# Performance work log

Hardware: AMD Instinct MI355X
Metric: run time of the kernel (lower is better)

The kernel has to match this reference:

```python
import math
import jax, jax.numpy as jnp
import numpy as np

HEADS = 8


def setup_inputs() -> dict:
    key = jax.random.key(0)
    k1, k2, k3 = jax.random.split(key, 3)
    b, n, a, dim = 1, 256, 256, 512
    init_scale = 0.02
    x = jax.random.normal(k1, (b, n, a, dim), dtype=jnp.float32)
    w_qkv = jax.random.normal(k2, (dim, 3 * dim), dtype=jnp.float32) * init_scale
    b_qkv = jnp.zeros((3 * dim,), dtype=jnp.float32)
    w_proj = jax.random.normal(k3, (dim, dim), dtype=jnp.float32) * init_scale
    b_proj = jnp.zeros((dim,), dtype=jnp.float32)
    return {"x": x, "w_qkv": w_qkv, "b_qkv": b_qkv, "w_proj": w_proj, "b_proj": b_proj}


def reference(x, w_qkv, b_qkv, w_proj, b_proj):
    b, n, a, dim = x.shape
    dh = dim // HEADS
    scale = 1.0 / math.sqrt(math.sqrt(dh))
    qkv = jnp.einsum('bnad,de->bnae', x, w_qkv) + b_qkv  # [b,n,a,3*dim]
    qkv = qkv.reshape(b, n, a, HEADS, 3 * dh)
    q, k, v = jnp.split(qkv, 3, axis=-1)  # each [b,n,a,h,dh]
    # scores over the 'a' axis, independent per (b, n, head)
    sim = jnp.einsum('bnihd,bnjhd->bnhij', q * scale, k * scale)
    attn = jax.nn.softmax(sim, axis=-1)
    out = jnp.einsum('bnhij,bnjhd->bnihd', attn, v).reshape(b, n, a, dim)
    return jnp.einsum('bnad,de->bnae', out, w_proj) + b_proj
```

## Files before the change

### kernel.cpp

```cpp
#include <hip/hip_runtime.h>

typedef unsigned short u16;
typedef unsigned int u32;
typedef __bf16 bf16x8 __attribute__((ext_vector_type(8)));
typedef float f32x4 __attribute__((ext_vector_type(4)));

__device__ __forceinline__ u16 f2b(float f) {
  u32 u = __builtin_bit_cast(u32, f);
  u32 r = (u + 0x7fffu + ((u >> 16) & 1u)) >> 16;
  return (u16)r;
}
__device__ __forceinline__ bf16x8 ld_frag(const u16* p) {
  uint4 v = *(const uint4*)p;
  return __builtin_bit_cast(bf16x8, v);
}
__device__ __forceinline__ void async_lds16(const u16* g, u16* lds) {
  __builtin_amdgcn_global_load_lds(
      (const __attribute__((address_space(1))) void*)g,
      (__attribute__((address_space(3))) void*)lds, 16, 0, 0);
}
__device__ __forceinline__ void wait_lds() { __builtin_amdgcn_s_waitcnt(0xc07f); }

__global__ __launch_bounds__(256) void convert_f32_bf16(const float* __restrict__ in,
                                                        u16* __restrict__ out) {
  long i = ((long)blockIdx.x * 256 + threadIdx.x) * 8;
  float4 a = *(const float4*)(in + i);
  float4 b = *(const float4*)(in + i + 4);
  union { uint4 v; u16 e[8]; } u;
  u.e[0] = f2b(a.x); u.e[1] = f2b(a.y); u.e[2] = f2b(a.z); u.e[3] = f2b(a.w);
  u.e[4] = f2b(b.x); u.e[5] = f2b(b.y); u.e[6] = f2b(b.z); u.e[7] = f2b(b.w);
  *(uint4*)(out + i) = u.v;
}

__global__ __launch_bounds__(256) void transpose_w(const float* __restrict__ W,
                                                   u16* __restrict__ Wt,
                                                   int K, int N) {
  __shared__ alignas(16) u16 T[64][80];
  const int n0 = blockIdx.x * 64, k0 = blockIdx.y * 64;
  const int t = threadIdx.x;
  {
    int kk = t >> 3, c = t & 7;
#pragma unroll
    for (int rr = 0; rr < 2; ++rr) {
      int kr = kk + rr * 32;
      const float* src = W + (long)(k0 + kr) * N + n0 + c * 8;
      float4 a = *(const float4*)src;
      float4 b = *(const float4*)(src + 4);
      u16* dst = &T[kr][c * 8];
      dst[0] = f2b(a.x); dst[1] = f2b(a.y); dst[2] = f2b(a.z); dst[3] = f2b(a.w);
      dst[4] = f2b(b.x); dst[5] = f2b(b.y); dst[6] = f2b(b.z); dst[7] = f2b(b.w);
    }
  }
  __syncthreads();
  {
    int nn = t >> 3, kc = t & 7;
#pragma unroll
    for (int rr = 0; rr < 2; ++rr) {
      int nr = nn + rr * 32;
      union { uint4 v; u16 e[8]; } u;
#pragma unroll
      for (int i = 0; i < 8; ++i) u.e[i] = T[kc * 8 + i][nr];
      *(uint4*)(Wt + (long)(n0 + nr) * K + k0 + kc * 8) = u.v;
    }
  }
}

template <bool OUT_F32>
__global__ __launch_bounds__(256) void gemm_bt(const u16* __restrict__ A,
                                               const u16* __restrict__ Bt,
                                               const float* __restrict__ bias,
                                               void* __restrict__ Cv,
                                               int M, int N, int K) {
  __shared__ alignas(16) u16 As[128 * 32];
  __shared__ alignas(16) u16 Bs[128 * 32];
  const int tid = threadIdx.x;
  const int lane = tid & 63, wave = tid >> 6;
  const int quad = lane >> 4, ln = lane & 15;
  const int wm = wave & 1, wn = wave >> 1;
  const long m0 = (long)blockIdx.y * 128;
  const long n0 = (long)blockIdx.x * 128;

  f32x4 zero = {0.f, 0.f, 0.f, 0.f};
  f32x4 acc[4][4];
#pragma unroll
  for (int i = 0; i < 4; ++i)
#pragma unroll
    for (int j = 0; j < 4; ++j) acc[i][j] = zero;

  const int c1 = tid + 256;
  const int rowA0 = tid >> 2, colA0 = (tid & 3) * 8;
  const int rowA1 = c1 >> 2, colA1 = (c1 & 3) * 8;
  u16* ldsA0 = &As[wave * 512];
  u16* ldsA1 = &As[2048 + wave * 512];
  u16* ldsB0 = &Bs[wave * 512];
  u16* ldsB1 = &Bs[2048 + wave * 512];

  for (int k0 = 0; k0 < K; k0 += 32) {
    async_lds16(A + (m0 + rowA0) * K + k0 + colA0, ldsA0);
    async_lds16(A + (m0 + rowA1) * K + k0 + colA1, ldsA1);
    async_lds16(Bt + (n0 + rowA0) * K + k0 + colA0, ldsB0);
    async_lds16(Bt + (n0 + rowA1) * K + k0 + colA1, ldsB1);
    __builtin_amdgcn_s_waitcnt(0x0f70);
    __syncthreads();
    bf16x8 af[4], bfr[4];
#pragma unroll
    for (int mt = 0; mt < 4; ++mt)
      af[mt] = ld_frag(&As[(wm * 64 + mt * 16 + ln) * 32 + quad * 8]);
#pragma unroll
    for (int nt = 0; nt < 4; ++nt)
      bfr[nt] = ld_frag(&Bs[(wn * 64 + nt * 16 + ln) * 32 + quad * 8]);
#pragma unroll
    for (int mt = 0; mt < 4; ++mt)
#pragma unroll
      for (int nt = 0; nt < 4; ++nt)
        acc[mt][nt] = __builtin_amdgcn_mfma_f32_16x16x32_bf16(af[mt], bfr[nt], acc[mt][nt], 0, 0, 0);
    __syncthreads();
  }

  if (OUT_F32) {
#pragma unroll
    for (int nt = 0; nt < 4; ++nt) {
      long coln = n0 + wn * 64 + nt * 16 + ln;
      float bv = bias[coln];
#pragma unroll
      for (int mt = 0; mt < 4; ++mt) {
        long rowb = m0 + wm * 64 + mt * 16 + quad * 4;
#pragma unroll
        for (int r = 0; r < 4; ++r)
          ((float*)Cv)[(rowb + r) * N + coln] = acc[mt][nt][r] + bv;
      }
    }
  } else {
    u16* buf = (wm == 0) ? As : Bs;
    for (int mt = 0; mt < 4; ++mt) {
      __syncthreads();
#pragma unroll
      for (int nt = 0; nt < 4; ++nt) {
        long coln = n0 + wn * 64 + nt * 16 + ln;
        float bv = bias[coln];
#pragma unroll
        for (int r = 0; r < 4; ++r)
          buf[(quad * 4 + r) * 136 + wn * 64 + nt * 16 + ln] = f2b(acc[mt][nt][r] + bv);
      }
      __syncthreads();
#pragma unroll
      for (int it = 0; it < 2; ++it) {
        int cid = it * 256 + tid;
        int bufi = cid >> 8, row = (cid >> 4) & 15, ch = cid & 15;
        const u16* sb = bufi ? Bs : As;
        uint4 v = *(const uint4*)&sb[row * 136 + ch * 8];
        *(uint4*)&((u16*)Cv)[(m0 + (long)bufi * 64 + mt * 16 + row) * N + n0 + ch * 8] = v;
      }
    }
  }
}

__global__ __launch_bounds__(256, 2) void attn_fused(const u16* __restrict__ qkv,
                                                     u16* __restrict__ out) {
  __shared__ alignas(16) u16 Ks[256 * 64];
  __shared__ alignas(16) u16 Vt[64 * 256];
  const int h = blockIdx.x;
  const long n = blockIdx.y;
  const int tid = threadIdx.x;
  const int lane = tid & 63, wave = tid >> 6;
  const int quad = lane >> 4, ln = lane & 15;
  const u16* base = qkv + (n * 256) * 1536 + h * 192;

  auto stageK = [&]() {
    int c = tid & 7, jb = tid >> 3;
#pragma unroll
    for (int rr = 0; rr < 8; ++rr) {
      int j = jb + rr * 32;
      uint4 v = *(const uint4*)(base + (long)j * 1536 + 64 + c * 8);
      *(uint4*)&Ks[j * 64 + ((c ^ (j & 7)) * 8)] = v;
    }
  };
  stageK();
  {
    int p = tid & 7, jb = tid >> 3;
#pragma unroll
    for (int rr = 0; rr < 8; ++rr) {
      int j = jb + rr * 32;
      union { uint4 v; u16 e[8]; } u;
      u.v = *(const uint4*)(base + (long)j * 1536 + 128 + p * 8);
      int cj = j >> 3, jl = j & 7;
#pragma unroll
      for (int i = 0; i < 8; ++i) {
        int d = p * 8 + i;
        int key = (p ^ i) & 7;
        Vt[d * 256 + ((cj ^ key) * 8) + jl] = u.e[i];
      }
    }
  }
  __syncthreads();

  u16* Pw = &Ks[wave * 2176];
  f32x4 zero = {0.f, 0.f, 0.f, 0.f};

  for (int s = 0; s < 2; ++s) {
    const int row0 = wave * 64 + s * 32;
    bf16x8 qa[2][2];
#pragma unroll
    for (int mt = 0; mt < 2; ++mt)
#pragma unroll
      for (int kc = 0; kc < 2; ++kc)
        qa[mt][kc] = ld_frag(base + (long)(row0 + mt * 16 + ln) * 1536 + kc * 32 + quad * 8);

    f32x4 sacc[2][16];
#pragma unroll
    for (int mt = 0; mt < 2; ++mt)
#pragma unroll
      for (int jt = 0; jt < 16; ++jt) sacc[mt][jt] = zero;

#pragma unroll
    for (int jt = 0; jt < 16; ++jt) {
#pragma unroll
      for (int kc = 0; kc < 2; ++kc) {
        bf16x8 kb = ld_frag(&Ks[(jt * 16 + ln) * 64 + (((kc * 4 + quad) ^ (ln & 7)) * 8)]);
        sacc[0][jt] = __builtin_amdgcn_mfma_f32_16x16x32_bf16(qa[0][kc], kb, sacc[0][jt], 0, 0, 0);
        sacc[1][jt] = __builtin_amdgcn_mfma_f32_16x16x32_bf16(qa[1][kc], kb, sacc[1][jt], 0, 0, 0);
      }
    }
    __syncthreads();

#pragma unroll
    for (int mt = 0; mt < 2; ++mt) {
      float linv[4];
#pragma unroll
      for (int r = 0; r < 4; ++r) {
        float mx = -3.0e38f;
#pragma unroll
        for (int jt = 0; jt < 16; ++jt) mx = fmaxf(mx, sacc[mt][jt][r]);
        mx = fmaxf(mx, __shfl_xor(mx, 1));
        mx = fmaxf(mx, __shfl_xor(mx, 2));
        mx = fmaxf(mx, __shfl_xor(mx, 4));
        mx = fmaxf(mx, __shfl_xor(mx, 8));
        float l = 0.f;
#pragma unroll
        for (int jt = 0; jt < 16; ++jt) {
          float p = __expf((sacc[mt][jt][r] - mx) * 0.125f);
          sacc[mt][jt][r] = p;
          l += p;
        }
        l += __shfl_xor(l, 1);
        l += __shfl_xor(l, 2);
        l += __shfl_xor(l, 4);
        l += __shfl_xor(l, 8);
        linv[r] = 1.0f / l;
      }

      f32x4 oacc[4];
#pragma unroll
      for (int dt = 0; dt < 4; ++dt) oacc[dt] = zero;
#pragma unroll
      for (int jh = 0; jh < 2; ++jh) {
#pragma unroll
        for (int jl = 0; jl < 8; ++jl) {
          int jt = jh * 8 + jl;
#pragma unroll
          for (int r = 0; r < 4; ++r)
            Pw[(quad * 4 + r) * 136 + jl * 16 + ln] = f2b(sacc[mt][jt][r]);
        }
        wait_lds();
#pragma unroll
        for (int jcl = 0; jcl < 4; ++jcl) {
          bf16x8 pa = ld_frag(&Pw[ln * 136 + jcl * 32 + quad * 8]);
          int cjb = (jh * 4 + jcl) * 4 + quad;
#pragma unroll
          for (int dt = 0; dt < 4; ++dt) {
            int d = dt * 16 + ln;
            int key = ((d >> 3) ^ d) & 7;
            bf16x8 vb = ld_frag(&Vt[d * 256 + ((cjb ^ key) * 8)]);
            oacc[dt] = __builtin_amdgcn_mfma_f32_16x16x32_bf16(pa, vb, oacc[dt], 0, 0, 0);
          }
        }
      }
#pragma unroll
      for (int dt = 0; dt < 4; ++dt)
#pragma unroll
        for (int r = 0; r < 4; ++r)
          Pw[(quad * 4 + r) * 136 + dt * 16 + ln] = f2b(oacc[dt][r] * linv[r]);
      wait_lds();
#pragma unroll
      for (int it = 0; it < 2; ++it) {
        int cid = it * 64 + lane;
        int row = cid >> 3, ch = cid & 7;
        uint4 v = *(const uint4*)&Pw[row * 136 + ch * 8];
        *(uint4*)&out[(n * 256 + row0 + mt * 16 + row) * 512 + h * 64 + ch * 8] = v;
      }
    }
    __syncthreads();
    if (s == 0) {
      stageK();
      __syncthreads();
    }
  }
}

extern "C" void kernel_launch(void* const* d_in, const int* in_sizes, int n_in,
                              void* d_out, int out_size, void* d_ws, size_t ws_size,
                              hipStream_t stream) {
  const float* x      = (const float*)d_in[0];
  const float* w_qkv  = (const float*)d_in[1];
  const float* b_qkv  = (const float*)d_in[2];
  const float* w_proj = (const float*)d_in[3];
  const float* b_proj = (const float*)d_in[4];
  float* out = (float*)d_out;

  char* ws = (char*)d_ws;
  u16* xb   = (u16*)ws;
  u16* qkv  = (u16*)(ws + 67108864L);
  u16* attn = (u16*)(ws + 67108864L + 201326592L);
  u16* Wt1  = (u16*)(ws + 67108864L + 201326592L + 67108864L);
  u16* Wt2  = Wt1 + 1536 * 512;

  convert_f32_bf16<<<16384, 256, 0, stream>>>(x, xb);
  transpose_w<<<dim3(24, 8), 256, 0, stream>>>(w_qkv, Wt1, 512, 1536);
  transpose_w<<<dim3(8, 8), 256, 0, stream>>>(w_proj, Wt2, 512, 512);
  gemm_bt<false><<<dim3(12, 512), 256, 0, stream>>>(xb, Wt1, b_qkv, qkv, 65536, 1536, 512);
  attn_fused<<<dim3(8, 256), 256, 0, stream>>>(qkv, attn);
  gemm_bt<true><<<dim3(4, 512), 256, 0, stream>>>(attn, Wt2, b_proj, out, 65536, 512, 512);
}
```

Measured before the change: 559.2 us.

## Widen GEMM tiles to 128x256 and group blocks for L2 reuse

Enlarges the GEMM output tile from 128x128 to 128x256, so each wave computes 4x8 MFMA tiles. This doubles B-fragment reuse per A load and halves the number of A re-reads. A 1D grid is remapped so 8 consecutive M-tiles share the same N-column group, which is meant to improve L2 locality for the weight panel. The cost is more accumulator registers (128 floats) and more LDS (24KB), which may reduce occupancy.

```diff
diff --git a/kernel.cpp b/kernel.cpp
--- a/kernel.cpp
+++ b/kernel.cpp
@@ -65,62 +65,63 @@
   }
 }
 
-template <bool OUT_F32>
+template <bool OUT_F32, int NTB>
 __global__ __launch_bounds__(256) void gemm_bt(const u16* __restrict__ A,
                                                const u16* __restrict__ Bt,
                                                const float* __restrict__ bias,
                                                void* __restrict__ Cv,
                                                int M, int N, int K) {
-  __shared__ alignas(16) u16 As[128 * 32];
-  __shared__ alignas(16) u16 Bs[128 * 32];
+  __shared__ alignas(16) u16 S[12288];
+  u16* As = S;
+  u16* Bs = S + 4096;
   const int tid = threadIdx.x;
   const int lane = tid & 63, wave = tid >> 6;
   const int quad = lane >> 4, ln = lane & 15;
   const int wm = wave & 1, wn = wave >> 1;
-  const long m0 = (long)blockIdx.y * 128;
-  const long n0 = (long)blockIdx.x * 128;
+  const int id = blockIdx.x;
+  const int s = id / (8 * NTB), t = id % (8 * NTB);
+  const long m0 = (long)(s * 8 + (t & 7)) * 128;
+  const long n0 = (long)(t >> 3) * 256;
 
   f32x4 zero = {0.f, 0.f, 0.f, 0.f};
-  f32x4 acc[4][4];
+  f32x4 acc[4][8];
 #pragma unroll
   for (int i = 0; i < 4; ++i)
 #pragma unroll
-    for (int j = 0; j < 4; ++j) acc[i][j] = zero;
-
-  const int c1 = tid + 256;
-  const int rowA0 = tid >> 2, colA0 = (tid & 3) * 8;
-  const int rowA1 = c1 >> 2, colA1 = (c1 & 3) * 8;
-  u16* ldsA0 = &As[wave * 512];
-  u16* ldsA1 = &As[2048 + wave * 512];
-  u16* ldsB0 = &Bs[wave * 512];
-  u16* ldsB1 = &Bs[2048 + wave * 512];
+    for (int j = 0; j < 8; ++j) acc[i][j] = zero;
+
+  const int rowC = tid >> 2, colC = (tid & 3) * 8;
 
   for (int k0 = 0; k0 < K; k0 += 32) {
-    async_lds16(A + (m0 + rowA0) * K + k0 + colA0, ldsA0);
-    async_lds16(A + (m0 + rowA1) * K + k0 + colA1, ldsA1);
-    async_lds16(Bt + (n0 + rowA0) * K + k0 + colA0, ldsB0);
-    async_lds16(Bt + (n0 + rowA1) * K + k0 + colA1, ldsB1);
+#pragma unroll
+    for (int it = 0; it < 2; ++it)
+      async_lds16(A + (m0 + it * 64 + rowC) * K + k0 + colC,
+                  As + it * 2048 + wave * 512);
+#pragma unroll
+    for (int it = 0; it < 4; ++it)
+      async_lds16(Bt + (n0 + it * 64 + rowC) * K + k0 + colC,
+                  Bs + it * 2048 + wave * 512);
     __builtin_amdgcn_s_waitcnt(0x0f70);
     __syncthreads();
-    bf16x8 af[4], bfr[4];
+    bf16x8 af[4], bfr[8];
 #pragma unroll
     for (int mt = 0; mt < 4; ++mt)
       af[mt] = ld_frag(&As[(wm * 64 + mt * 16 + ln) * 32 + quad * 8]);
 #pragma unroll
-    for (int nt = 0; nt < 4; ++nt)
-      bfr[nt] = ld_frag(&Bs[(wn * 64 + nt * 16 + ln) * 32 + quad * 8]);
+    for (int nt = 0; nt < 8; ++nt)
+      bfr[nt] = ld_frag(&Bs[(wn * 128 + nt * 16 + ln) * 32 + quad * 8]);
 #pragma unroll
     for (int mt = 0; mt < 4; ++mt)
 #pragma unroll
-      for (int nt = 0; nt < 4; ++nt)
+      for (int nt = 0; nt < 8; ++nt)
         acc[mt][nt] = __builtin_amdgcn_mfma_f32_16x16x32_bf16(af[mt], bfr[nt], acc[mt][nt], 0, 0, 0);
     __syncthreads();
   }
 
   if (OUT_F32) {
 #pragma unroll
-    for (int nt = 0; nt < 4; ++nt) {
-      long coln = n0 + wn * 64 + nt * 16 + ln;
+    for (int nt = 0; nt < 8; ++nt) {
+      long coln = n0 + wn * 128 + nt * 16 + ln;
       float bv = bias[coln];
 #pragma unroll
       for (int mt = 0; mt < 4; ++mt) {
@@ -131,25 +132,24 @@
       }
     }
   } else {
-    u16* buf = (wm == 0) ? As : Bs;
     for (int mt = 0; mt < 4; ++mt) {
       __syncthreads();
-#pragma unroll
-      for (int nt = 0; nt < 4; ++nt) {
-        long coln = n0 + wn * 64 + nt * 16 + ln;
+      u16* buf = S + wm * 4224;
+#pragma unroll
+      for (int nt = 0; nt < 8; ++nt) {
+        long coln = n0 + wn * 128 + nt * 16 + ln;
         float bv = bias[coln];
 #pragma unroll
         for (int r = 0; r < 4; ++r)
-          buf[(quad * 4 + r) * 136 + wn * 64 + nt * 16 + ln] = f2b(acc[mt][nt][r] + bv);
+          buf[(quad * 4 + r) * 264 + wn * 128 + nt * 16 + ln] = f2b(acc[mt][nt][r] + bv);
       }
       __syncthreads();
 #pragma unroll
-      for (int it = 0; it < 2; ++it) {
+      for (int it = 0; it < 4; ++it) {
         int cid = it * 256 + tid;
-        int bufi = cid >> 8, row = (cid >> 4) & 15, ch = cid & 15;
-        const u16* sb = bufi ? Bs : As;
-        uint4 v = *(const uint4*)&sb[row * 136 + ch * 8];
-        *(uint4*)&((u16*)Cv)[(m0 + (long)bufi * 64 + mt * 16 + row) * N + n0 + ch * 8] = v;
+        int g = cid >> 9, row = (cid >> 5) & 15, ch = cid & 31;
+        uint4 v = *(const uint4*)&S[g * 4224 + row * 264 + ch * 8];
+        *(uint4*)&((u16*)Cv)[(m0 + g * 64 + mt * 16 + row) * N + n0 + ch * 8] = v;
       }
     }
   }
@@ -317,7 +317,7 @@
   convert_f32_bf16<<<16384, 256, 0, stream>>>(x, xb);
   transpose_w<<<dim3(24, 8), 256, 0, stream>>>(w_qkv, Wt1, 512, 1536);
   transpose_w<<<dim3(8, 8), 256, 0, stream>>>(w_proj, Wt2, 512, 512);
-  gemm_bt<false><<<dim3(12, 512), 256, 0, stream>>>(xb, Wt1, b_qkv, qkv, 65536, 1536, 512);
+  gemm_bt<false, 6><<<3072, 256, 0, stream>>>(xb, Wt1, b_qkv, qkv, 65536, 1536, 512);
   attn_fused<<<dim3(8, 256), 256, 0, stream>>>(qkv, attn);
-  gemm_bt<true><<<dim3(4, 512), 256, 0, stream>>>(attn, Wt2, b_proj, out, 65536, 512, 512);
-}
+  gemm_bt<true, 2><<<1024, 256, 0, stream>>>(attn, Wt2, b_proj, out, 65536, 512, 512);
+}
```

New measurement: 670.2 us. +19.8%, slower.
